# Optimization experiments

Measured on AMD Instinct MI355X. Metric: run time of the kernel, lower is better.

The kernel has to match this reference:

```python
import jax, jax.numpy as jnp
import numpy as np

B, S, T, E, H = 16, 96, 50, 128, 128
D2 = 2 * H
V = 32000
NGRAM = 2
ALPHA = 0.25


def _lstm(x, Wih, Whh, b, reverse=False):
    # x: [N, T, E] -> outputs [N, T, H], final h, c (PyTorch gate order i,f,g,o)
    xt = jnp.swapaxes(x, 0, 1)
    if reverse:
        xt = xt[::-1]
    n = x.shape[0]
    h = Whh.shape[1]
    init = (jnp.zeros((n, h), x.dtype), jnp.zeros((n, h), x.dtype))

    def step(carry, xin):
        hprev, cprev = carry
        g = xin @ Wih.T + hprev @ Whh.T + b
        i, f, gg, o = jnp.split(g, 4, axis=-1)
        c = jax.nn.sigmoid(f) * cprev + jax.nn.sigmoid(i) * jnp.tanh(gg)
        hnew = jax.nn.sigmoid(o) * jnp.tanh(c)
        return (hnew, c), hnew

    (hT, cT), outs = jax.lax.scan(step, init, xt)
    if reverse:
        outs = outs[::-1]
    return jnp.swapaxes(outs, 0, 1), hT, cT


def _gru(x, h, Wi, Wh, bi, bh):
    # PyTorch GRUCell, gate order r,z,n
    gi = x @ Wi.T + bi
    gh = h @ Wh.T + bh
    ir, iz, inn = jnp.split(gi, 3, axis=-1)
    hr, hz, hn = jnp.split(gh, 3, axis=-1)
    r = jax.nn.sigmoid(ir + hr)
    z = jax.nn.sigmoid(iz + hz)
    n = jnp.tanh(inn + r * hn)
    return (1.0 - z) * n + z * h


def _norm_scale(x):
    # (||x|| + alpha) / (||x|| + 1), detached as in the original
    v = jnp.linalg.norm(x, axis=1)
    return jax.lax.stop_gradient(((v + ALPHA) / (v + 1.0))[:, None])


def setup_inputs() -> dict:
    key = jax.random.key(0)
    ks = jax.random.split(key, 30)
    rn = lambda k, sh: jax.random.normal(k, sh, jnp.float32) * 0.05
    return {
        "enc_batch": jax.random.randint(ks[0], (B * S, T), 0, V),
        "struct_parent": jax.random.randint(ks[1], (B, S, S), 0, B * S + 1),
        "struct_child": jax.random.randint(ks[2], (B, S, S), 0, B * S + 1),
        "mask_emb": (jax.random.uniform(ks[3], (B, S, S, 1)) < 0.2).astype(jnp.float32),
        "emb_table": rn(ks[4], (V, E)),
        "Wih_f": rn(ks[5], (4 * H, E)), "Whh_f": rn(ks[6], (4 * H, H)), "b_f": rn(ks[7], (4 * H,)),
        "Wih_b": rn(ks[8], (4 * H, E)), "Whh_b": rn(ks[9], (4 * H, H)), "b_b": rn(ks[10], (4 * H,)),
        "Wc": rn(ks[11], (H, D2)), "bc": rn(ks[12], (H,)),
        "Whr": rn(ks[13], (H, D2)), "bhr": rn(ks[14], (H,)),
        "Wi_cp": rn(ks[15], (3 * D2, D2)), "Wh_cp": rn(ks[16], (3 * D2, D2)),
        "bi_cp": rn(ks[17], (3 * D2,)), "bh_cp": rn(ks[18], (3 * D2,)),
        "Wi_pc": rn(ks[19], (3 * D2, D2)), "Wh_pc": rn(ks[20], (3 * D2, D2)),
        "bi_pc": rn(ks[21], (3 * D2,)), "bh_pc": rn(ks[22], (3 * D2,)),
    }


def reference(enc_batch, struct_parent, struct_child, mask_emb, emb_table,
              Wih_f, Whh_f, b_f, Wih_b, Whh_b, b_b, Wc, bc, Whr, bhr,
              Wi_cp, Wh_cp, bi_cp, bh_cp, Wi_pc, Wh_pc, bi_pc, bh_pc):
    # Sentence encoder (bidirectional LSTM); dropout=0 -> identity
    emb = emb_table[enc_batch]                       # [B*S, T, E]
    _, hf, cf = _lstm(emb, Wih_f, Whh_f, b_f)
    _, hb, cb = _lstm(emb, Wih_b, Whh_b, b_b, reverse=True)
    c_red = jax.nn.relu(jnp.concatenate([cf, cb], 1) @ Wc.T + bc)
    h_red = jax.nn.relu(jnp.concatenate([hf, hb], 1) @ Whr.T + bhr)
    enc_states = jnp.concatenate([c_red, h_red], 1)  # [B*S, 2H]
    zero = jnp.zeros((1, D2), enc_states.dtype)
    hidden = jnp.concatenate([zero, enc_states], 0)  # [B*S+1, 2H]; row 0 = zero_emb

    # child -> parent message passing
    for _ in range(NGRAM):
        p = hidden[struct_parent].reshape(-1, D2)    # gather [B*S*S, 2H]
        c = hidden[struct_child].reshape(-1, D2)
        ch = _gru(c, p, Wi_cp, Wh_cp, bi_cp, bh_cp).reshape(B, S, S, D2)
        ch = (ch * mask_emb).sum(1).reshape(B * S, D2)
        ch = jnp.concatenate([zero, ch], 0)
        hidden = hidden + ch * _norm_scale(ch)

    # parent -> child message passing
    for _ in range(NGRAM):
        p = hidden[struct_parent].reshape(-1, D2)
        c = hidden[struct_child].reshape(-1, D2)
        ch = _gru(p, c, Wi_pc, Wh_pc, bi_pc, bh_pc).reshape(B, S, S, D2)
        ch = (ch * mask_emb).sum(2).reshape(B * S, D2)
        ch = jnp.concatenate([zero, ch], 0)
        hidden = hidden + ch * _norm_scale(ch)

    return hidden
```

## Files before the change

### kernel.cpp

```cpp
#include <hip/hip_runtime.h>

typedef unsigned short u16;
typedef __attribute__((ext_vector_type(8))) short bf8;
typedef __attribute__((ext_vector_type(4))) short s16x4;
typedef __attribute__((ext_vector_type(4))) float f32x4;
typedef __attribute__((ext_vector_type(4))) int   i32x4;

#define S_   96
#define T_   50
#define NSEQ 1536
#define NR   1537
#define XROW 520

__device__ __forceinline__ float bf2f(u16 u){ return __uint_as_float(((unsigned)u)<<16); }
__device__ __forceinline__ u16 f2bf(float f){
  unsigned u = __float_as_uint(f);
  u += 0x7fffu + ((u>>16)&1u);
  return (u16)(u>>16);
}
__device__ __forceinline__ float sigm(float x){
  return __builtin_amdgcn_rcpf(1.f + __expf(-x));
}
__device__ __forceinline__ float tanh_(float x){
  return 1.f - 2.f*__builtin_amdgcn_rcpf(__expf(2.f*x) + 1.f);
}
__device__ __forceinline__ void bar_lds(){
  asm volatile("s_waitcnt lgkmcnt(0)\n\ts_barrier" ::: "memory");
}

struct CvtArgs { const float* s[10]; u16* d[10]; };
__global__ __launch_bounds__(256) void prep_kernel(CvtArgs a,
    const int* __restrict__ par, const int* __restrict__ chi,
    const float* __restrict__ mask,
    int2* __restrict__ ent0, int* __restrict__ cnt0,
    int2* __restrict__ ent1, int* __restrict__ cnt1)
{
  if (blockIdx.x < 1088){
    int e = (blockIdx.x*256 + threadIdx.x)*4;
    if (e >= 1114112) return;
    int t, off;
    if (e < 262144){ t = e>>16; off = e & 65535; }
    else if (e < 327680){ int e2=e-262144; t = 4+(e2>>15); off = e2&32767; }
    else { int e3=e-327680; t = 6 + e3/196608; off = e3%196608; }
    int src = off;
    if (t < 4){
      int colp = off>>7, k = off&127;
      int orig = ((colp>>4)&3)*128 + ((colp>>6)<<4) + (colp&15);
      src = orig*128 + k;
    }
    f32x4 v = *reinterpret_cast<const f32x4*>(a.s[t]+src);
    s16x4 o;
    #pragma unroll
    for (int i=0;i<4;i++) o[i]=(short)f2bf(v[i]);
    *reinterpret_cast<s16x4*>(a.d[t]+off) = o;
  } else {
    const int rr = blockIdx.x - 1088;
    __shared__ int c0s, c1s;
    if (threadIdx.x==0){ c0s=0; c1s=0; }
    __syncthreads();
    const int l = threadIdx.x;
    if (l < S_){
      const int b = rr/S_, fx = rr%S_, base = b*S_*S_;
      int idx = base + l*S_ + fx;
      if (mask[idx] != 0.f){
        int p = atomicAdd(&c0s, 1);
        ent0[rr*S_ + p] = make_int2(chi[idx], par[idx]);
      }
      int jdx = base + fx*S_ + l;
      if (mask[jdx] != 0.f){
        int p = atomicAdd(&c1s, 1);
        ent1[rr*S_ + p] = make_int2(par[jdx], chi[jdx]);
      }
    }
    __syncthreads();
    if (threadIdx.x==0){ cnt0[rr]=c0s; cnt1[rr]=c1s; }
  }
}

__global__ __launch_bounds__(512, 2) void lstm_kernel(
    const int* __restrict__ enc, const float* __restrict__ emb,
    const u16* __restrict__ WihF, const u16* __restrict__ WhhF, const float* __restrict__ bF,
    const u16* __restrict__ WihB, const u16* __restrict__ WhhB, const float* __restrict__ bB,
    u16* __restrict__ c_cat, u16* __restrict__ h_cat)
{
  __shared__ short xh[16*XROW];
  __shared__ int   toks[16*T_];

  const int tid  = threadIdx.x;
  const int wave = tid>>6;
  const int lane = tid&63;
  const int dir  = blockIdx.y;
  const int s0   = blockIdx.x*16;

  const u16* Wih = dir ? WihB : WihF;
  const u16* Whh = dir ? WhhB : WhhF;
  const float* bb = dir ? bB  : bF;

  for (int i=tid; i<16*T_; i+=512)
    toks[i] = enc[(s0 + i/T_)*T_ + (i%T_)];

  const int mL   = lane&15;
  const int quad = lane>>4;
  const int kb   = quad*8;

  bf8 Breg[4][8];
  f32x4 bias4[4];
  #pragma unroll
  for (int n=0;n<4;n++){
    int colp = wave*64 + n*16 + mL;
    bias4[n] = *reinterpret_cast<const f32x4*>(bb + n*128 + wave*16 + quad*4);
    #pragma unroll
    for (int ks=0;ks<8;ks++){
      int k = ks*32 + kb;
      const u16* p = (k<128) ? (Wih + colp*128 + k) : (Whh + colp*128 + (k-128));
      Breg[n][ks] = *reinterpret_cast<const bf8*>(p);
      asm volatile("" : "+v"(Breg[n][ks]));
    }
  }

  if (tid<256){
    int r = tid>>4, c = tid&15;
    *reinterpret_cast<i32x4*>(&xh[r*XROW + 256 + c*8]) = (i32x4){0,0,0,0};
  }

  const int srow = tid>>5, schunk = tid&31;
  float cst[4] = {0.f,0.f,0.f,0.f};
  float hst[4] = {0.f,0.f,0.f,0.f};

  __syncthreads();

  {
    int tok = toks[srow*T_ + (dir ? (T_-1) : 0)];
    f32x4 xv = *reinterpret_cast<const f32x4*>(emb + tok*128 + schunk*4);
    s16x4 xp;
    #pragma unroll
    for (int i=0;i<4;i++) xp[i]=(short)f2bf(xv[i]);
    *reinterpret_cast<s16x4*>(&xh[srow*XROW + schunk*4]) = xp;
  }
  f32x4 xv1, xv2;
  {
    int tok1 = toks[srow*T_ + (dir ? (T_-2) : 1)];
    xv1 = *reinterpret_cast<const f32x4*>(emb + tok1*128 + schunk*4);
    int tok2 = toks[srow*T_ + (dir ? (T_-3) : 2)];
    xv2 = *reinterpret_cast<const f32x4*>(emb + tok2*128 + schunk*4);
  }
  __syncthreads();

  for (int t=0;t<T_;t++){
    const int cb = t&1, nb2 = (t+1)&1;
    if (t+1 < T_){
      s16x4 xp;
      #pragma unroll
      for (int i=0;i<4;i++) xp[i]=(short)f2bf(xv1[i]);
      *reinterpret_cast<s16x4*>(&xh[srow*XROW + nb2*128 + schunk*4]) = xp;
    }
    xv1 = xv2;
    if (t+3 < T_){
      int tok = toks[srow*T_ + (dir ? (T_-4-t) : (t+3))];
      xv2 = *reinterpret_cast<const f32x4*>(emb + tok*128 + schunk*4);
    }

    f32x4 acc[4];
    #pragma unroll
    for (int i=0;i<4;i++) acc[i] = (f32x4){0.f,0.f,0.f,0.f};
    #pragma unroll
    for (int ks=0;ks<8;ks++){
      int k = ks*32 + kb;
      int off = (k<128) ? (cb*128 + k) : (256 + cb*128 + (k-128));
      bf8 b = *reinterpret_cast<const bf8*>(&xh[mL*XROW + off]);
      #pragma unroll
      for (int n=0;n<4;n++)
        acc[n] = __builtin_amdgcn_mfma_f32_16x16x32_bf16(Breg[n][ks], b, acc[n], 0,0,0);
    }

    s16x4 hp;
    #pragma unroll
    for (int i=0;i<4;i++){
      float gi_ = acc[0][i]+bias4[0][i];
      float gf_ = acc[1][i]+bias4[1][i];
      float gg_ = acc[2][i]+bias4[2][i];
      float go_ = acc[3][i]+bias4[3][i];
      float c = sigm(gf_)*cst[i] + sigm(gi_)*tanh_(gg_);
      float h = sigm(go_)*tanh_(c);
      cst[i]=c; hst[i]=h;
      hp[i] = (short)f2bf(h);
    }
    *reinterpret_cast<s16x4*>(&xh[mL*XROW + 256 + nb2*128 + wave*16 + quad*4]) = hp;
    bar_lds();
  }

  {
    const int ch = wave*16 + quad*4;
    const int gs = s0 + mL;
    s16x4 cp_, hp_;
    #pragma unroll
    for (int i=0;i<4;i++){ cp_[i]=(short)f2bf(cst[i]); hp_[i]=(short)f2bf(hst[i]); }
    *reinterpret_cast<s16x4*>(c_cat + gs*256 + dir*128 + ch) = cp_;
    *reinterpret_cast<s16x4*>(h_cat + gs*256 + dir*128 + ch) = hp_;
  }
}

__global__ __launch_bounds__(256) void reduce_kernel(
    const u16* __restrict__ c_cat, const u16* __restrict__ h_cat,
    const u16* __restrict__ Wc, const float* __restrict__ bc,
    const u16* __restrict__ Whr, const float* __restrict__ bhr,
    float* __restrict__ hidf, u16* __restrict__ hidb)
{
  const int tid=threadIdx.x, wave=tid>>6, lane=tid&63;
  const int mL=lane&15, quad=lane>>4, kb=quad*8;
  const int m0 = blockIdx.x*64;
  const u16* A    = (wave<2) ? c_cat : h_cat;
  const u16* W    = (wave<2) ? Wc  : Whr;
  const float* bv = (wave<2) ? bc  : bhr;
  const int nb    = (wave&1)*64;
  const int obase = (wave<2) ? 0 : 128;

  f32x4 acc[4][4];
  #pragma unroll
  for (int mt=0;mt<4;mt++)
    #pragma unroll
    for (int nt=0;nt<4;nt++) acc[mt][nt] = (f32x4){0.f,0.f,0.f,0.f};

  #pragma unroll
  for (int ks=0;ks<8;ks++){
    int k = ks*32 + kb;
    bf8 bfr[4];
    #pragma unroll
    for (int nt=0;nt<4;nt++)
      bfr[nt] = *reinterpret_cast<const bf8*>(W + (nb+nt*16+mL)*256 + k);
    #pragma unroll
    for (int mt=0;mt<4;mt++){
      bf8 a = *reinterpret_cast<const bf8*>(A + (m0+mt*16+mL)*256 + k);
      #pragma unroll
      for (int nt=0;nt<4;nt++)
        acc[mt][nt] = __builtin_amdgcn_mfma_f32_16x16x32_bf16(a, bfr[nt], acc[mt][nt], 0,0,0);
    }
  }
  const int row0 = quad*4;
  float biasv[4];
  #pragma unroll
  for (int nt=0;nt<4;nt++) biasv[nt] = bv[nb+nt*16+mL];
  #pragma unroll
  for (int mt=0;mt<4;mt++){
    #pragma unroll
    for (int nt=0;nt<4;nt++){
      int col = obase + nb + nt*16 + mL;
      #pragma unroll
      for (int i=0;i<4;i++){
        int r = m0 + mt*16 + row0 + i;
        float v = fmaxf(acc[mt][nt][i] + biasv[nt], 0.f);
        hidf[(r+1)*256 + col] = v;
        hidb[(r+1)*256 + col] = f2bf(v);
      }
    }
  }
  if (blockIdx.x==0 && tid<64){
    #pragma unroll
    for (int j=0;j<4;j++){ hidf[tid*4+j] = 0.f; hidb[tid*4+j] = 0; }
  }
}

__global__ __launch_bounds__(256) void gates_gemm_kernel(
    const u16* __restrict__ hidb,
    const u16* __restrict__ Wi, const u16* __restrict__ Wh,
    const float* __restrict__ bi, const float* __restrict__ bh,
    u16* __restrict__ gi, u16* __restrict__ gh)
{
  const int tid=threadIdx.x, wave=tid>>6, lane=tid&63;
  const int mL=lane&15, quad=lane>>4, kb=quad*8;
  const int m0 = blockIdx.x*32;
  const int n0 = blockIdx.y*256 + wave*64;
  const bool isI = (n0 < 768);
  const u16* W    = isI ? Wi : Wh;
  const float* bv = isI ? bi : bh;
  u16* out        = isI ? gi : gh;
  const int nbc   = isI ? n0 : (n0-768);

  int arow[2];
  #pragma unroll
  for (int mt=0;mt<2;mt++) arow[mt] = min(m0+mt*16+mL, NR-1);

  f32x4 acc[2][4];
  #pragma unroll
  for (int mt=0;mt<2;mt++)
    #pragma unroll
    for (int nt=0;nt<4;nt++) acc[mt][nt] = (f32x4){0.f,0.f,0.f,0.f};

  #pragma unroll
  for (int ks=0;ks<8;ks++){
    int k = ks*32 + kb;
    bf8 bfr[4];
    #pragma unroll
    for (int nt=0;nt<4;nt++)
      bfr[nt] = *reinterpret_cast<const bf8*>(W + (nbc+nt*16+mL)*256 + k);
    #pragma unroll
    for (int mt=0;mt<2;mt++){
      bf8 a = *reinterpret_cast<const bf8*>(hidb + arow[mt]*256 + k);
      #pragma unroll
      for (int nt=0;nt<4;nt++)
        acc[mt][nt] = __builtin_amdgcn_mfma_f32_16x16x32_bf16(a, bfr[nt], acc[mt][nt], 0,0,0);
    }
  }
  const int row0 = quad*4;
  float biasv[4];
  #pragma unroll
  for (int nt=0;nt<4;nt++) biasv[nt] = bv[nbc+nt*16+mL];
  #pragma unroll
  for (int mt=0;mt<2;mt++){
    #pragma unroll
    for (int nt=0;nt<4;nt++){
      #pragma unroll
      for (int i=0;i<4;i++){
        int r = m0 + mt*16 + row0 + i;
        if (r < NR)
          out[r*768 + nbc + nt*16 + mL] = f2bf(acc[mt][nt][i] + biasv[nt]);
      }
    }
  }
}

__global__ __launch_bounds__(512) void pair_kernel(
    const u16* __restrict__ gi, const u16* __restrict__ gh,
    const float* __restrict__ hin,
    float* __restrict__ hout, u16* __restrict__ bout, float* __restrict__ dout,
    const int2* __restrict__ ent, const int* __restrict__ cnt)
{
  const int r = blockIdx.x;
  const int tid = threadIdx.x, wave = tid>>6, lane = tid&63;
  __shared__ float part[8][260];
  __shared__ float ssum[4];
  if (r==0){
    if (tid<256){
      hout[tid]=0.f; bout[tid]=0;
      if (dout) dout[tid]=0.f;
    }
    return;
  }
  const int rr = r-1;
  const int n  = cnt[rr];
  const int2* e = ent + rr*S_;
  const int ch0 = lane*4;

  float a0=0.f, a1=0.f, a2=0.f, a3=0.f;
  for (int k=wave; k<n; k+=8){
    int2 pr = e[k];
    const u16* gx = gi + pr.x*768 + ch0;
    const u16* gy = gh + pr.y*768 + ch0;
    s16x4 vi0 = *reinterpret_cast<const s16x4*>(gx);
    s16x4 vi1 = *reinterpret_cast<const s16x4*>(gx+256);
    s16x4 vi2 = *reinterpret_cast<const s16x4*>(gx+512);
    s16x4 vh0 = *reinterpret_cast<const s16x4*>(gy);
    s16x4 vh1 = *reinterpret_cast<const s16x4*>(gy+256);
    s16x4 vh2 = *reinterpret_cast<const s16x4*>(gy+512);
    f32x4 hv  = *reinterpret_cast<const f32x4*>(hin + pr.y*256 + ch0);
    float o[4];
    #pragma unroll
    for (int i=0;i<4;i++){
      float rg = sigm(bf2f((u16)vi0[i]) + bf2f((u16)vh0[i]));
      float zg = sigm(bf2f((u16)vi1[i]) + bf2f((u16)vh1[i]));
      float ng = tanh_(bf2f((u16)vi2[i]) + rg*bf2f((u16)vh2[i]));
      o[i] = (1.f-zg)*ng + zg*hv[i];
    }
    a0 += o[0]; a1 += o[1]; a2 += o[2]; a3 += o[3];
  }
  *reinterpret_cast<f32x4*>(&part[wave][ch0]) = (f32x4){a0,a1,a2,a3};
  __syncthreads();

  if (tid < 256){
    float tot = part[0][tid] + part[1][tid] + part[2][tid] + part[3][tid]
              + part[4][tid] + part[5][tid] + part[6][tid] + part[7][tid];
    part[0][tid] = tot;
    float sq = tot*tot;
    #pragma unroll
    for (int off=32; off>0; off>>=1) sq += __shfl_xor(sq, off, 64);
    if (lane==0) ssum[wave] = sq;
  }
  __syncthreads();
  if (tid < 256){
    float tot = part[0][tid];
    float v  = sqrtf(ssum[0]+ssum[1]+ssum[2]+ssum[3]);
    float sc = (v + 0.25f)*__builtin_amdgcn_rcpf(v + 1.f);
    float nv = hin[r*256 + tid] + tot*sc;
    hout[r*256 + tid] = nv;
    bout[r*256 + tid] = f2bf(nv);
    if (dout) dout[r*256 + tid] = nv;
  }
}

extern "C" void kernel_launch(void* const* d_in, const int* in_sizes, int n_in,
                              void* d_out, int out_size, void* d_ws, size_t ws_size,
                              hipStream_t stream)
{
  const int*   enc  = (const int*)  d_in[0];
  const int*   spar = (const int*)  d_in[1];
  const int*   schi = (const int*)  d_in[2];
  const float* mask = (const float*)d_in[3];
  const float* emb  = (const float*)d_in[4];
  const float* WihF = (const float*)d_in[5];
  const float* WhhF = (const float*)d_in[6];
  const float* bF   = (const float*)d_in[7];
  const float* WihB = (const float*)d_in[8];
  const float* WhhB = (const float*)d_in[9];
  const float* bB   = (const float*)d_in[10];
  const float* Wc   = (const float*)d_in[11];
  const float* bc   = (const float*)d_in[12];
  const float* Whr  = (const float*)d_in[13];
  const float* bhr  = (const float*)d_in[14];
  const float* WiCP = (const float*)d_in[15];
  const float* WhCP = (const float*)d_in[16];
  const float* biCP = (const float*)d_in[17];
  const float* bhCP = (const float*)d_in[18];
  const float* WiPC = (const float*)d_in[19];
  const float* WhPC = (const float*)d_in[20];
  const float* biPC = (const float*)d_in[21];
  const float* bhPC = (const float*)d_in[22];

  char* ws = (char*)d_ws;
  u16*   c_cat = (u16*)  (ws + 0);
  u16*   h_cat = (u16*)  (ws + 786432);
  float* hf0   = (float*)(ws + 1572864);
  float* hf1   = (float*)(ws + 3146752);
  u16*   hb    = (u16*)  (ws + 4720640);
  u16*   gi    = (u16*)  (ws + 5507584);
  u16*   gh    = (u16*)  (ws + 7868416);
  u16*   wbf   = (u16*)  (ws + 10229248);
  int2*  ent0  = (int2*) (ws + 12457472);
  int2*  ent1  = (int2*) (ws + 13637120);
  int*   cnt0  = (int*)  (ws + 14816768);
  int*   cnt1  = (int*)  (ws + 14822912);
  float* out   = (float*)d_out;

  u16* bWihF = wbf + 0;
  u16* bWhhF = wbf + 65536;
  u16* bWihB = wbf + 131072;
  u16* bWhhB = wbf + 196608;
  u16* bWc   = wbf + 262144;
  u16* bWhr  = wbf + 294912;
  u16* bWiCP = wbf + 327680;
  u16* bWhCP = wbf + 524288;
  u16* bWiPC = wbf + 720896;
  u16* bWhPC = wbf + 917504;

  CvtArgs ca;
  ca.s[0]=WihF; ca.s[1]=WhhF; ca.s[2]=WihB; ca.s[3]=WhhB;
  ca.s[4]=Wc;   ca.s[5]=Whr;
  ca.s[6]=WiCP; ca.s[7]=WhCP; ca.s[8]=WiPC; ca.s[9]=WhPC;
  ca.d[0]=bWihF; ca.d[1]=bWhhF; ca.d[2]=bWihB; ca.d[3]=bWhhB;
  ca.d[4]=bWc;   ca.d[5]=bWhr;
  ca.d[6]=bWiCP; ca.d[7]=bWhCP; ca.d[8]=bWiPC; ca.d[9]=bWhPC;
  prep_kernel<<<dim3(1088+NSEQ), dim3(256), 0, stream>>>(
      ca, spar, schi, mask, ent0, cnt0, ent1, cnt1);

  lstm_kernel<<<dim3(96,2), dim3(512), 0, stream>>>(
      enc, emb, bWihF,bWhhF,bF, bWihB,bWhhB,bB, c_cat, h_cat);
  reduce_kernel<<<dim3(24), dim3(256), 0, stream>>>(
      c_cat,h_cat, bWc,bc,bWhr,bhr, hf0,hb);

  float* hfb[2] = {hf0,hf1};
  int cur = 0;
  for (int it=0; it<4; it++){
    const u16* Wi   = (it<2)?bWiCP:bWiPC;
    const u16* Wh   = (it<2)?bWhCP:bWhPC;
    const float* bi = (it<2)?biCP:biPC;
    const float* bh = (it<2)?bhCP:bhPC;
    int nxt = cur^1;
    gates_gemm_kernel<<<dim3(49,6), dim3(256), 0, stream>>>(
        hb, Wi,Wh,bi,bh, gi,gh);
    pair_kernel<<<dim3(NR), dim3(512), 0, stream>>>(
        gi,gh, hfb[cur], hfb[nxt], hb,
        (it==3)?out:(float*)nullptr,
        (it<2)?ent0:ent1, (it<2)?cnt0:cnt1);
    cur = nxt;
  }
}
```

Measured before the change: 330.2 us.

## Precompute next-step input projection off the LSTM recurrence critical path

Splits the per-step LSTM gate matmul into an input part (x @ Wih) and a recurrent part (h @ Whh). The input part for step t+1 is computed during step t, after the current recurrent MFMAs, so only the 4 recurrent K-slices sit on the serial dependency chain. The x-tile buffering is reworked to match: two steps are preloaded and the prefetch distance changes. Manual round-to-nearest bf16 conversion is also replaced with the packed v_cvt_pk_bf16_f32 instruction, which costs extra live accumulator registers and reorders LDS buffer usage.

```diff
diff --git a/kernel.cpp b/kernel.cpp
--- a/kernel.cpp
+++ b/kernel.cpp
@@ -5,6 +5,7 @@
 typedef __attribute__((ext_vector_type(4))) short s16x4;
 typedef __attribute__((ext_vector_type(4))) float f32x4;
 typedef __attribute__((ext_vector_type(4))) int   i32x4;
+typedef __attribute__((ext_vector_type(2))) int   i32x2;
 
 #define S_   96
 #define T_   50
@@ -17,6 +18,9 @@
   unsigned u = __float_as_uint(f);
   u += 0x7fffu + ((u>>16)&1u);
   return (u16)(u>>16);
+}
+__device__ __forceinline__ int cvtpk(float lo, float hi){
+  int r; asm("v_cvt_pk_bf16_f32 %0, %1, %2" : "=v"(r) : "v"(lo), "v"(hi)); return r;
 }
 __device__ __forceinline__ float sigm(float x){
   return __builtin_amdgcn_rcpf(1.f + __expf(-x));
@@ -49,10 +53,10 @@
       src = orig*128 + k;
     }
     f32x4 v = *reinterpret_cast<const f32x4*>(a.s[t]+src);
-    s16x4 o;
-    #pragma unroll
-    for (int i=0;i<4;i++) o[i]=(short)f2bf(v[i]);
-    *reinterpret_cast<s16x4*>(a.d[t]+off) = o;
+    i32x2 o;
+    o[0] = cvtpk(v[0], v[1]);
+    o[1] = cvtpk(v[2], v[3]);
+    *reinterpret_cast<i32x2*>(a.d[t]+off) = o;
   } else {
     const int rr = blockIdx.x - 1088;
     __shared__ int c0s, c1s;
@@ -130,50 +134,73 @@
   __syncthreads();
 
   {
-    int tok = toks[srow*T_ + (dir ? (T_-1) : 0)];
-    f32x4 xv = *reinterpret_cast<const f32x4*>(emb + tok*128 + schunk*4);
-    s16x4 xp;
-    #pragma unroll
-    for (int i=0;i<4;i++) xp[i]=(short)f2bf(xv[i]);
-    *reinterpret_cast<s16x4*>(&xh[srow*XROW + schunk*4]) = xp;
-  }
-  f32x4 xv1, xv2;
+    int tok0 = toks[srow*T_ + (dir ? (T_-1) : 0)];
+    f32x4 x0 = *reinterpret_cast<const f32x4*>(emb + tok0*128 + schunk*4);
+    int tok1 = toks[srow*T_ + (dir ? (T_-2) : 1)];
+    f32x4 x1 = *reinterpret_cast<const f32x4*>(emb + tok1*128 + schunk*4);
+    i32x2 p0; p0[0]=cvtpk(x0[0],x0[1]); p0[1]=cvtpk(x0[2],x0[3]);
+    i32x2 p1; p1[0]=cvtpk(x1[0],x1[1]); p1[1]=cvtpk(x1[2],x1[3]);
+    *reinterpret_cast<i32x2*>(&xh[srow*XROW +       schunk*4]) = p0;
+    *reinterpret_cast<i32x2*>(&xh[srow*XROW + 128 + schunk*4]) = p1;
+  }
+  f32x4 xvA, xvB;
   {
-    int tok1 = toks[srow*T_ + (dir ? (T_-2) : 1)];
-    xv1 = *reinterpret_cast<const f32x4*>(emb + tok1*128 + schunk*4);
-    int tok2 = toks[srow*T_ + (dir ? (T_-3) : 2)];
-    xv2 = *reinterpret_cast<const f32x4*>(emb + tok2*128 + schunk*4);
+    int tA = toks[srow*T_ + (dir ? (T_-3) : 2)];
+    xvA = *reinterpret_cast<const f32x4*>(emb + tA*128 + schunk*4);
+    int tB = toks[srow*T_ + (dir ? (T_-4) : 3)];
+    xvB = *reinterpret_cast<const f32x4*>(emb + tB*128 + schunk*4);
   }
   __syncthreads();
 
+  f32x4 accx[4];
+  #pragma unroll
+  for (int n=0;n<4;n++) accx[n] = (f32x4){0.f,0.f,0.f,0.f};
+  #pragma unroll
+  for (int ks=0;ks<4;ks++){
+    bf8 b = *reinterpret_cast<const bf8*>(&xh[mL*XROW + ks*32 + kb]);
+    #pragma unroll
+    for (int n=0;n<4;n++)
+      accx[n] = __builtin_amdgcn_mfma_f32_16x16x32_bf16(Breg[n][ks], b, accx[n], 0,0,0);
+  }
+  bar_lds();
+
   for (int t=0;t<T_;t++){
-    const int cb = t&1, nb2 = (t+1)&1;
+    const int cb = t&1, nb = cb^1;
+
+    f32x4 acc[4];
+    #pragma unroll
+    for (int n=0;n<4;n++) acc[n] = accx[n];
+    #pragma unroll
+    for (int ks=0;ks<4;ks++){
+      bf8 b = *reinterpret_cast<const bf8*>(&xh[mL*XROW + 256 + cb*128 + ks*32 + kb]);
+      #pragma unroll
+      for (int n=0;n<4;n++)
+        acc[n] = __builtin_amdgcn_mfma_f32_16x16x32_bf16(Breg[n][4+ks], b, acc[n], 0,0,0);
+    }
+
+    if (t+2 < T_){
+      i32x2 p; p[0]=cvtpk(xvA[0],xvA[1]); p[1]=cvtpk(xvA[2],xvA[3]);
+      *reinterpret_cast<i32x2*>(&xh[srow*XROW + cb*128 + schunk*4]) = p;
+    }
+    xvA = xvB;
+    if (t+4 < T_){
+      int tok = toks[srow*T_ + (dir ? (T_-5-t) : (t+4))];
+      xvB = *reinterpret_cast<const f32x4*>(emb + tok*128 + schunk*4);
+    }
+
     if (t+1 < T_){
-      s16x4 xp;
-      #pragma unroll
-      for (int i=0;i<4;i++) xp[i]=(short)f2bf(xv1[i]);
-      *reinterpret_cast<s16x4*>(&xh[srow*XROW + nb2*128 + schunk*4]) = xp;
-    }
-    xv1 = xv2;
-    if (t+3 < T_){
-      int tok = toks[srow*T_ + (dir ? (T_-4-t) : (t+3))];
-      xv2 = *reinterpret_cast<const f32x4*>(emb + tok*128 + schunk*4);
-    }
-
-    f32x4 acc[4];
-    #pragma unroll
-    for (int i=0;i<4;i++) acc[i] = (f32x4){0.f,0.f,0.f,0.f};
-    #pragma unroll
-    for (int ks=0;ks<8;ks++){
-      int k = ks*32 + kb;
-      int off = (k<128) ? (cb*128 + k) : (256 + cb*128 + (k-128));
-      bf8 b = *reinterpret_cast<const bf8*>(&xh[mL*XROW + off]);
-      #pragma unroll
-      for (int n=0;n<4;n++)
-        acc[n] = __builtin_amdgcn_mfma_f32_16x16x32_bf16(Breg[n][ks], b, acc[n], 0,0,0);
-    }
-
-    s16x4 hp;
+      #pragma unroll
+      for (int n=0;n<4;n++) accx[n] = (f32x4){0.f,0.f,0.f,0.f};
+      #pragma unroll
+      for (int ks=0;ks<4;ks++){
+        bf8 b = *reinterpret_cast<const bf8*>(&xh[mL*XROW + nb*128 + ks*32 + kb]);
+        #pragma unroll
+        for (int n=0;n<4;n++)
+          accx[n] = __builtin_amdgcn_mfma_f32_16x16x32_bf16(Breg[n][ks], b, accx[n], 0,0,0);
+      }
+    }
+
+    float hv4[4];
     #pragma unroll
     for (int i=0;i<4;i++){
       float gi_ = acc[0][i]+bias4[0][i];
@@ -182,21 +209,22 @@
       float go_ = acc[3][i]+bias4[3][i];
       float c = sigm(gf_)*cst[i] + sigm(gi_)*tanh_(gg_);
       float h = sigm(go_)*tanh_(c);
-      cst[i]=c; hst[i]=h;
-      hp[i] = (short)f2bf(h);
-    }
-    *reinterpret_cast<s16x4*>(&xh[mL*XROW + 256 + nb2*128 + wave*16 + quad*4]) = hp;
+      cst[i]=c; hst[i]=h; hv4[i]=h;
+    }
+    i32x2 hp;
+    hp[0]=cvtpk(hv4[0],hv4[1]); hp[1]=cvtpk(hv4[2],hv4[3]);
+    *reinterpret_cast<i32x2*>(&xh[mL*XROW + 256 + nb*128 + wave*16 + quad*4]) = hp;
     bar_lds();
   }
 
   {
     const int ch = wave*16 + quad*4;
     const int gs = s0 + mL;
-    s16x4 cp_, hp_;
-    #pragma unroll
-    for (int i=0;i<4;i++){ cp_[i]=(short)f2bf(cst[i]); hp_[i]=(short)f2bf(hst[i]); }
-    *reinterpret_cast<s16x4*>(c_cat + gs*256 + dir*128 + ch) = cp_;
-    *reinterpret_cast<s16x4*>(h_cat + gs*256 + dir*128 + ch) = hp_;
+    i32x2 cp_, hp_;
+    cp_[0]=cvtpk(cst[0],cst[1]); cp_[1]=cvtpk(cst[2],cst[3]);
+    hp_[0]=cvtpk(hst[0],hst[1]); hp_[1]=cvtpk(hst[2],hst[3]);
+    *reinterpret_cast<i32x2*>(c_cat + gs*256 + dir*128 + ch) = cp_;
+    *reinterpret_cast<i32x2*>(h_cat + gs*256 + dir*128 + ch) = hp_;
   }
 }
 
```

Result: faster. 322.2 us (-2.4%).
